# Optimization experiments

Measured on AMD Instinct MI355X. Metric: run time of the kernel, lower is better.

The kernel has to match this reference:

```python
import jax, jax.numpy as jnp
import numpy as np

B, LAT, H, O, T, NPART = 256, 512, 1024, 128, 100, 2


def _lin(x, w, b):
    return x @ w.T + b


def _lrelu(x):
    return jnp.where(x > 0, x, 0.01 * x)


def setup_inputs() -> dict:
    key = jax.random.key(0)
    ks = jax.random.split(key, 32)
    s = 0.02
    def n(k, shape):
        return jax.random.normal(k, shape, dtype=jnp.float32) * s
    return {
        "encoder_outputs": jax.random.normal(ks[0], (B, LAT), dtype=jnp.float32),
        "encoder_hidden": jax.random.normal(ks[1], (B, LAT), dtype=jnp.float32),
        "start_token": jax.random.normal(ks[2], (1, O), dtype=jnp.float32),
        "lat2hid_w": n(ks[3], (H, LAT)), "lat2hid_b": n(ks[4], (H,)),
        "lat2hid2_w": n(ks[5], (H, LAT)), "lat2hid2_b": n(ks[6], (H,)),
        "emb_fc_w": n(ks[7], (H, O)), "emb_fc_b": n(ks[8], (H,)),
        "W_ih": n(ks[9], (4 * H, H)), "W_hh": n(ks[10], (4 * H, H)),
        "b_ih": n(ks[11], (4 * H,)), "b_hh": n(ks[12], (4 * H,)),
        "out_w": n(ks[13], (O, H)), "out_b": n(ks[14], (O,)),
        "fc_seq_w": n(ks[15], (H, LAT)), "fc_seq_b": n(ks[16], (H,)),
        "fc_seq2_w": n(ks[17], (1, H)), "fc_seq2_b": n(ks[18], (1,)),
        "fc_mass_w": n(ks[19], (H, LAT)), "fc_mass_b": n(ks[20], (H,)),
        "fc_mass2_w": n(ks[21], (H, H)), "fc_mass2_b": n(ks[22], (H,)),
        "fc_mass3_w": n(ks[23], (NPART, H)), "fc_mass3_b": n(ks[24], (NPART,)),
        "seq_len": T,
    }


def reference(encoder_outputs, encoder_hidden, start_token,
              lat2hid_w, lat2hid_b, lat2hid2_w, lat2hid2_b,
              emb_fc_w, emb_fc_b, W_ih, W_hh, b_ih, b_hh,
              out_w, out_b, fc_seq_w, fc_seq_b, fc_seq2_w, fc_seq2_b,
              fc_mass_w, fc_mass_b, fc_mass2_w, fc_mass2_b,
              fc_mass3_w, fc_mass3_b, seq_len):
    batch = encoder_hidden.shape[0]
    # initial LSTM state: LeakyReLU(Linear(encoder_hidden))
    h0 = _lrelu(_lin(encoder_hidden, lat2hid_w, lat2hid_b))   # [B,H]
    c0 = _lrelu(_lin(encoder_hidden, lat2hid2_w, lat2hid2_b))  # [B,H]
    # embedded start token, repeated over batch
    x0 = jnp.broadcast_to(_lin(start_token, emb_fc_w, emb_fc_b), (batch, h0.shape[1]))

    def step(carry, _):
        h, c, x = carry
        xr = jax.nn.relu(x)  # forward_step applies relu to the input
        gates = _lin(xr, W_ih, b_ih) + _lin(h, W_hh, b_hh)  # [B,4H], torch gate order i,f,g,o
        i, f, g, o = jnp.split(gates, 4, axis=-1)
        c = jax.nn.sigmoid(f) * c + jax.nn.sigmoid(i) * jnp.tanh(g)
        h = jax.nn.sigmoid(o) * jnp.tanh(c)
        # LSTM output h is fed back as next input (before the `out` projection)
        return (h, c, h), h

    (hT, cT, _), hs = jax.lax.scan(step, (h0, c0, x0), None, length=seq_len)
    decoder_outputs = _lin(hs.transpose(1, 0, 2), out_w, out_b)  # [B,T,O]

    num = jax.nn.relu(_lin(_lrelu(_lin(encoder_outputs, fc_seq_w, fc_seq_b)), fc_seq2_w, fc_seq2_b))  # [B,1]
    m = _lrelu(_lin(encoder_outputs, fc_mass_w, fc_mass_b))
    m = _lrelu(_lin(m, fc_mass2_w, fc_mass2_b))
    mass = jax.nn.softmax(_lin(m, fc_mass3_w, fc_mass3_b), axis=-1)  # [B,num_part]
    return (decoder_outputs, hT[None], cT[None], num, mass)
```

## Files before the change

kernel.cpp:

```cpp
#include <hip/hip_runtime.h>

#define BD 256
#define HD 1024
#define KC 2048
#define LATD 512
#define OD 128
#define TS 100

typedef __attribute__((ext_vector_type(8))) short s16x8;
typedef __attribute__((ext_vector_type(4))) float f32x4;

__device__ __forceinline__ float b2f(short s) {
  return __uint_as_float(((unsigned)(unsigned short)s) << 16);
}
__device__ __forceinline__ short f2b(float f) {
  unsigned u = __float_as_uint(f);
  u += 0x7fff + ((u >> 16) & 1);
  return (short)(u >> 16);
}
__device__ __forceinline__ float sigm(float x) { return 1.f / (1.f + __expf(-x)); }
__device__ __forceinline__ float tanh_f(float x) { return 1.f - 2.f / (__expf(2.f * x) + 1.f); }

__device__ __forceinline__ size_t hf_idx(int m, int kh) {
  int kc = kh >> 3;
  int q2 = kc >> 6, it = (kc >> 2) & 15, qq = kc & 3;
  int mt = m >> 4, r = m & 15;
  return (((size_t)(mt * 32 + q2 * 16 + it)) * 64 + qq * 16 + r) * 8 + (kh & 7);
}

__device__ __forceinline__ s16x8 relu8(s16x8 v) {
  s16x8 o;
#pragma unroll
  for (int e = 0; e < 8; ++e) o[e] = v[e] > 0 ? v[e] : (short)0;
  return o;
}


__global__ __launch_bounds__(256) void cvt8_k(const float* __restrict__ in,
                                              short* __restrict__ out) {
  int i = (blockIdx.x * 256 + threadIdx.x) * 8;
  f32x4 a = *(const f32x4*)(in + i), b = *(const f32x4*)(in + i + 4);
  s16x8 o;
#pragma unroll
  for (int e = 0; e < 4; ++e) { o[e] = f2b(a[e]); o[4 + e] = f2b(b[e]); }
  *(s16x8*)(out + i) = o;
}

__global__ __launch_bounds__(256) void wrep_k(const float* __restrict__ Wih,
                                              const float* __restrict__ Whh,
                                              short* __restrict__ Wt) {
  int i = blockIdx.x * 256 + threadIdx.x;
  int lan = i & 15, quad = (i >> 4) & 3, kit = (i >> 6) & 63, bn = i >> 12;
  int g = bn >> 6, bx = bn & 63;
  int n = g * HD + bx * 16 + lan;
  int k = kit * 32 + quad * 8;
  const float* src = (k < HD) ? (Wih + (size_t)n * HD + k)
                              : (Whh + (size_t)n * HD + (k - HD));
  f32x4 a = *(const f32x4*)src, b = *(const f32x4*)(src + 4);
  s16x8 o;
#pragma unroll
  for (int e = 0; e < 4; ++e) { o[e] = f2b(a[e]); o[4 + e] = f2b(b[e]); }
  *(s16x8*)(Wt + (size_t)i * 8) = o;
}

__global__ __launch_bounds__(256) void bsum_k(const float* __restrict__ bi,
                                              const float* __restrict__ bh,
                                              float* __restrict__ bs) {
  int i = blockIdx.x * 256 + threadIdx.x;
  bs[i] = bi[i] + bh[i];
}

__global__ __launch_bounds__(256) void x0_k(const float* __restrict__ st,
                                            const float* __restrict__ W,
                                            const float* __restrict__ bias,
                                            short* __restrict__ xrow) {
  int j = blockIdx.x * 256 + threadIdx.x;
  float acc = 0.f;
  for (int k = 0; k < OD; ++k) acc += st[k] * W[j * OD + k];
  acc += bias[j];
  xrow[j] = f2b(acc > 0.f ? acc : 0.f);
}

__global__ __launch_bounds__(256) void xg_k(const short* __restrict__ xrow,
                                            const float* __restrict__ Wih,
                                            float* __restrict__ xg) {
  int l = threadIdx.x & 63, w = threadIdx.x >> 6;
  int j = blockIdx.x * 4 + w;
  const float* row = Wih + (size_t)j * HD + l * 16;
  float acc = 0.f;
#pragma unroll
  for (int c = 0; c < 16; ++c) acc += b2f(xrow[l * 16 + c]) * row[c];
  for (int off = 32; off; off >>= 1) acc += __shfl_down(acc, off);
  if (l == 0) xg[j] = acc;
}

__global__ void zero_ctr_k(unsigned* __restrict__ c) { c[threadIdx.x] = 0u; }

template <int K, bool IN_BF16, int MODE>
__global__ __launch_bounds__(256) void fc_mfma(const void* __restrict__ in_,
                                               const float* __restrict__ W,
                                               const float* __restrict__ bias,
                                               void* __restrict__ out_,
                                               int ostride, int ooff) {
  const int tid = threadIdx.x;
  const int w = tid >> 6, lan = tid & 15, quad = (tid & 63) >> 4;
  const int n0 = blockIdx.x * 64;
  const int m0 = blockIdx.y * 64;
  const int arow = m0 + w * 16 + lan;
  f32x4 acc[4] = {};
  for (int k0 = 0; k0 < K; k0 += 32) {
    const int ka = k0 + quad * 8;
    s16x8 af;
    if (IN_BF16) {
      af = *(const s16x8*)((const short*)in_ + arow * K + ka);
    } else {
      const float* ap = (const float*)in_ + arow * K + ka;
      f32x4 a0 = *(const f32x4*)ap, a1 = *(const f32x4*)(ap + 4);
#pragma unroll
      for (int e = 0; e < 4; ++e) { af[e] = f2b(a0[e]); af[4 + e] = f2b(a1[e]); }
    }
#pragma unroll
    for (int nf = 0; nf < 4; ++nf) {
      const float* bp = W + (n0 + nf * 16 + lan) * K + ka;
      f32x4 b0 = *(const f32x4*)bp, b1 = *(const f32x4*)(bp + 4);
      s16x8 bf;
#pragma unroll
      for (int e = 0; e < 4; ++e) { bf[e] = f2b(b0[e]); bf[4 + e] = f2b(b1[e]); }
      acc[nf] = __builtin_amdgcn_mfma_f32_16x16x32_bf16(af, bf, acc[nf], 0, 0, 0);
    }
  }
#pragma unroll
  for (int nf = 0; nf < 4; ++nf) {
    int col = n0 + nf * 16 + lan;
    float bb = bias[col];
#pragma unroll
    for (int j = 0; j < 4; ++j) {
      int m = m0 + w * 16 + quad * 4 + j;
      float v = acc[nf][j] + bb;
      v = v > 0.f ? v : 0.01f * v;
      if (MODE == 0)
        ((float*)out_)[m * 1024 + col] = v;
      else if (MODE == 1)
        ((short*)out_)[m * ostride + ooff + col] = f2b(v);
      else
        ((short*)out_)[hf_idx(m, col)] = f2b(v);
    }
  }
}

__global__ __launch_bounds__(256) void num_k(const float* __restrict__ n1,
                                             const float* __restrict__ w2,
                                             const float* __restrict__ b2,
                                             float* __restrict__ out) {
  int l = threadIdx.x & 63, w = threadIdx.x >> 6;
  int m = blockIdx.x * 4 + w;
  const float* r = n1 + m * HD + l * 16;
  const float* wv = w2 + l * 16;
  float acc = 0.f;
#pragma unroll
  for (int c = 0; c < 4; ++c) {
    f32x4 a = *(const f32x4*)(r + c * 4), b = *(const f32x4*)(wv + c * 4);
#pragma unroll
    for (int e = 0; e < 4; ++e) acc += a[e] * b[e];
  }
  for (int off = 32; off; off >>= 1) acc += __shfl_down(acc, off);
  if (l == 0) {
    float v = acc + b2[0];
    out[m] = v > 0.f ? v : 0.f;
  }
}

__global__ __launch_bounds__(256) void mass_k(const short* __restrict__ m2,
                                              const float* __restrict__ w3,
                                              const float* __restrict__ b3,
                                              float* __restrict__ out) {
  int l = threadIdx.x & 63, w = threadIdx.x >> 6;
  int m = blockIdx.x * 4 + w;
  const short* r = m2 + m * HD + l * 16;
  s16x8 v0 = *(const s16x8*)r, v1 = *(const s16x8*)(r + 8);
  float z0 = 0.f, z1 = 0.f;
#pragma unroll
  for (int e = 0; e < 8; ++e) {
    float a = b2f(v0[e]), b = b2f(v1[e]);
    z0 += a * w3[l * 16 + e] + b * w3[l * 16 + 8 + e];
    z1 += a * w3[HD + l * 16 + e] + b * w3[HD + l * 16 + 8 + e];
  }
  for (int off = 32; off; off >>= 1) {
    z0 += __shfl_down(z0, off);
    z1 += __shfl_down(z1, off);
  }
  if (l == 0) {
    z0 += b3[0]; z1 += b3[1];
    float mx = fmaxf(z0, z1);
    float e0 = __expf(z0 - mx), e1 = __expf(z1 - mx);
    float s = e0 + e1;
    out[m * 2] = e0 / s;
    out[m * 2 + 1] = e1 / s;
  }
}


#define MF(a, b, c) __builtin_amdgcn_mfma_f32_16x16x32_bf16(a, b, c, 0, 0, 0)

typedef __attribute__((address_space(1))) const void gas_void;
typedef __attribute__((address_space(3))) void las_void;

__device__ __forceinline__ void grid_bar(unsigned* slots, unsigned epoch, int bx) {
  asm volatile("s_waitcnt vmcnt(0)" ::: "memory");
  __syncthreads();
  if (threadIdx.x == 0)
    __hip_atomic_store(slots + bx, epoch, __ATOMIC_RELAXED, __HIP_MEMORY_SCOPE_AGENT);
  if (threadIdx.x < 64) {
    while (!__all(__hip_atomic_load(slots + (int)threadIdx.x, __ATOMIC_RELAXED,
                                    __HIP_MEMORY_SCOPE_AGENT) >= epoch))
      __builtin_amdgcn_s_sleep(1);
  }
  __syncthreads();
}

__global__ __launch_bounds__(512, 2) void lstm_persist(
    short* __restrict__ hA, short* __restrict__ hB, const float* __restrict__ cbuf,
    const short* __restrict__ Wt, const float* __restrict__ bsum,
    const float* __restrict__ xg, short* __restrict__ hsC,
    const short* __restrict__ outw, const float* __restrict__ outb,
    float* __restrict__ dout, float* __restrict__ o_h, float* __restrict__ o_c,
    unsigned* ctr, int CH) {
  __shared__ __align__(16) short sm[65536];

  const int tid = threadIdx.x;
  const int w = tid >> 6, l = tid & 63;
  const int w4 = w & 3, gp = w >> 2;
  const int bx = blockIdx.x, by = blockIdx.y;
  const int q = l >> 4, r = l & 15;
  const int q2 = w4 & 1;
  const int sr = (w4 >> 1) + 2 * gp;

  s16x8 W[32];
#pragma unroll
  for (int it = 0; it < 16; ++it)
#pragma unroll
    for (int gi = 0; gi < 2; ++gi) {
      const int g = gp * 2 + gi;
      W[it * 2 + gi] =
          *(const s16x8*)(Wt + (((size_t)(g * 64 + bx) * 64 + w4 * 16 + it) * 64 + l) * 8);
    }
#pragma unroll
  for (int i = 0; i < 32; ++i) asm volatile("" : "+v"(W[i]));

  const int mloc0 = tid >> 4, hc = tid & 15;
  const int chh = bx * 16 + hc;
  const float bs0 = bsum[chh], bs1 = bsum[HD + chh];
  const float bs2 = bsum[2 * HD + chh], bs3 = bsum[3 * HD + chh];
  const float xg0 = xg[chh], xg1 = xg[HD + chh];
  const float xg2 = xg[2 * HD + chh], xg3 = xg[3 * HD + chh];
  int idxA[2];
  size_t hIdx[2];
  float creg[2];
#pragma unroll
  for (int cc2 = 0; cc2 < 2; ++cc2) {
    const int mg = by * 64 + mloc0 + cc2 * 32;
    idxA[cc2] = mg * HD + chh;
    hIdx[cc2] = hf_idx(mg, chh);
    creg[cc2] = cbuf[idxA[cc2]];
  }

  float* red = (float*)sm;
  unsigned* s1 = ctr + by * 128;
  unsigned* s2 = s1 + 64;
  int tslot = 0;
  unsigned pcnt = 0;

  for (int t = 0; t < TS; ++t) {
    const short* src = (t & 1) ? hB : hA;
    short* dst = (t & 1) ? hA : hB;

    f32x4 c00 = {}, c01 = {}, c10 = {}, c11 = {};
    f32x4 c20 = {}, c21 = {}, c30 = {}, c31 = {};

#pragma unroll
    for (int j = 0; j < 16; ++j) {
      const int fi = sr * 16 + j;
      const int it = fi >> 2, mtl = fi & 3;
      const short* g = src + ((size_t)((by * 4 + mtl) * 32 + q2 * 16 + it)) * 512 + (size_t)l * 8;
      __builtin_amdgcn_global_load_lds((gas_void*)g,
                                       (las_void*)(sm + q2 * 32768 + fi * 512), 16, 0, 17);
    }
    asm volatile("s_waitcnt vmcnt(0)" ::: "memory");
    __builtin_amdgcn_s_barrier();

    if (t > 0 || w4 >= 2) {
      const short* cb = sm + q2 * 32768;
#pragma unroll
      for (int it = 0; it < 16; ++it) {
        const short* fb = cb + it * 2048 + l * 8;
        s16x8 a0 = *(const s16x8*)(fb);
        s16x8 a1 = *(const s16x8*)(fb + 512);
        s16x8 a2 = *(const s16x8*)(fb + 1024);
        s16x8 a3 = *(const s16x8*)(fb + 1536);
        if (w4 < 2) { a0 = relu8(a0); a1 = relu8(a1); a2 = relu8(a2); a3 = relu8(a3); }
        const s16x8 w0 = W[it * 2], w1 = W[it * 2 + 1];
        c00 = MF(a0, w0, c00); c01 = MF(a0, w1, c01);
        c10 = MF(a1, w0, c10); c11 = MF(a1, w1, c11);
        c20 = MF(a2, w0, c20); c21 = MF(a2, w1, c21);
        c30 = MF(a3, w0, c30); c31 = MF(a3, w1, c31);
      }
    }
    __builtin_amdgcn_s_barrier();

    {
      float* base = red + (size_t)(w * 64 + l) * 4;
      *(f32x4*)(base + 0 * 2048) = c00;
      *(f32x4*)(base + 1 * 2048) = c01;
      *(f32x4*)(base + 2 * 2048) = c10;
      *(f32x4*)(base + 3 * 2048) = c11;
      *(f32x4*)(base + 4 * 2048) = c20;
      *(f32x4*)(base + 5 * 2048) = c21;
      *(f32x4*)(base + 6 * 2048) = c30;
      *(f32x4*)(base + 7 * 2048) = c31;
    }
    __syncthreads();

#pragma unroll
    for (int cc2 = 0; cc2 < 2; ++cc2) {
      const int mloc = mloc0 + cc2 * 32;
      const int mtl = mloc >> 4, qq = (mloc & 15) >> 2, jj = mloc & 3;
      const int lane = qq * 16 + hc;
      float g4[4];
#pragma unroll
      for (int g = 0; g < 4; ++g) {
        const int s = mtl * 2 + (g & 1);
        const int wv = (g >> 1) * 4;
        float sum = 0.f;
#pragma unroll
        for (int k2 = 0; k2 < 4; ++k2)
          sum += red[(size_t)(s * 512 + (wv + k2) * 64 + lane) * 4 + jj];
        g4[g] = sum;
      }
      float gi_ = g4[0] + bs0;
      float gf = g4[1] + bs1;
      float gg = g4[2] + bs2;
      float go = g4[3] + bs3;
      if (t == 0) { gi_ += xg0; gf += xg1; gg += xg2; go += xg3; }
      float cn = sigm(gf) * creg[cc2] + sigm(gi_) * tanh_f(gg);
      creg[cc2] = cn;
      float h = sigm(go) * tanh_f(cn);
      short h16 = f2b(h);
      __hip_atomic_store(dst + hIdx[cc2], h16, __ATOMIC_RELAXED, __HIP_MEMORY_SCOPE_AGENT);
      __hip_atomic_store(hsC + (size_t)tslot * BD * HD + idxA[cc2], h16,
                         __ATOMIC_RELAXED, __HIP_MEMORY_SCOPE_AGENT);
      if (t == TS - 1) { o_h[idxA[cc2]] = h; o_c[idxA[cc2]] = cn; }
    }
    if (++tslot == CH) tslot = 0;

    grid_bar(s1, (unsigned)(t + 1), bx);

    if (tslot == 0) {
      if (bx < 2 * CH) {
        const int tloc = bx >> 1, nj = bx & 1;
        const int tglob = t + 1 - CH + tloc;
        const short* hsrc = hsC + (size_t)tloc * BD * HD + (size_t)by * 64 * HD;
        const int amt = w & 3, nfh = w >> 2;
        f32x4 p0 = {}, p1 = {};
#pragma unroll
        for (int cc = 0; cc < 2; ++cc) {
#pragma unroll
          for (int j = 0; j < 8; ++j) {
            const int fi = w * 8 + j;
            const int it = fi >> 2, ml = fi & 3;
            const short* g = hsrc + (size_t)(ml * 16 + r) * HD + (cc * 16 + it) * 32 + q * 8;
            __builtin_amdgcn_global_load_lds((gas_void*)g, (las_void*)(sm + fi * 512), 16, 0, 17);
          }
          asm volatile("s_waitcnt vmcnt(0)" ::: "memory");
          __syncthreads();
#pragma unroll
          for (int itl = 0; itl < 16; ++itl) {
            const short* fb = sm + itl * 2048 + amt * 512 + l * 8;
            s16x8 a = *(const s16x8*)(fb);
            const int kk = (cc * 16 + itl) * 32 + q * 8;
            s16x8 b0 = *(const s16x8*)(outw + (size_t)(nj * 64 + nfh * 32 + r) * HD + kk);
            s16x8 b1 = *(const s16x8*)(outw + (size_t)(nj * 64 + nfh * 32 + 16 + r) * HD + kk);
            p0 = MF(a, b0, p0);
            p1 = MF(a, b1, p1);
          }
          __syncthreads();
        }
#pragma unroll
        for (int f2 = 0; f2 < 2; ++f2) {
          const int col = nj * 64 + nfh * 32 + f2 * 16 + r;
          const float bb = outb[col];
          const f32x4 pa = f2 ? p1 : p0;
#pragma unroll
          for (int j2 = 0; j2 < 4; ++j2) {
            const int brow = by * 64 + amt * 16 + q * 4 + j2;
            dout[((size_t)brow * TS + tglob) * OD + col] = pa[j2] + bb;
          }
        }
      }
      ++pcnt;
      grid_bar(s2, pcnt, bx);
    }
  }
}

extern "C" void kernel_launch(void* const* d_in, const int* in_sizes, int n_in,
                              void* d_out, int out_size, void* d_ws, size_t ws_size,
                              hipStream_t stream) {
  static const int exp_sizes[26] = {
      131072, 131072, 128, 524288, 1024, 524288, 1024, 131072, 1024,
      4194304, 4194304, 4096, 4096, 131072, 128, 524288, 1024, 1024, 1,
      524288, 1024, 1048576, 1024, 2048, 2, 1};
  if (n_in < 26) return;
  for (int i = 0; i < 26; ++i)
    if (in_sizes[i] != exp_sizes[i]) return;

  const float* enc_out = (const float*)d_in[0];
  const float* enc_hid = (const float*)d_in[1];
  const float* start_tok = (const float*)d_in[2];
  const float* l2h_w = (const float*)d_in[3];
  const float* l2h_b = (const float*)d_in[4];
  const float* l2h2_w = (const float*)d_in[5];
  const float* l2h2_b = (const float*)d_in[6];
  const float* emb_w = (const float*)d_in[7];
  const float* emb_b = (const float*)d_in[8];
  const float* Wih_f = (const float*)d_in[9];
  const float* Whh_f = (const float*)d_in[10];
  const float* bih = (const float*)d_in[11];
  const float* bhh = (const float*)d_in[12];
  const float* outw_f = (const float*)d_in[13];
  const float* outb = (const float*)d_in[14];
  const float* seq_w = (const float*)d_in[15];
  const float* seq_b = (const float*)d_in[16];
  const float* seq2_w = (const float*)d_in[17];
  const float* seq2_b = (const float*)d_in[18];
  const float* mass_w = (const float*)d_in[19];
  const float* mass_b = (const float*)d_in[20];
  const float* mass2_w = (const float*)d_in[21];
  const float* mass2_b = (const float*)d_in[22];
  const float* mass3_w = (const float*)d_in[23];
  const float* mass3_b = (const float*)d_in[24];

  char* p = (char*)d_ws;
  float* c_buf = (float*)p;  p += (size_t)BD * HD * 4;
  float* bsum = (float*)p;   p += (size_t)4 * HD * 4;
  float* xg = (float*)p;     p += (size_t)4 * HD * 4;
  float* n1 = (float*)p;     p += (size_t)BD * HD * 4;
  short* m1 = (short*)p;     p += (size_t)BD * HD * 2;
  short* m2 = (short*)p;     p += (size_t)BD * HD * 2;
  short* xrow = (short*)p;   p += (size_t)HD * 2;
  short* hA = (short*)p;     p += (size_t)BD * HD * 2;
  short* hB = (short*)p;     p += (size_t)BD * HD * 2;
  short* Wt = (short*)p;     p += (size_t)4 * HD * KC * 2;
  short* outw = (short*)p;   p += (size_t)OD * HD * 2;
  unsigned* ctrs = (unsigned*)p; p += 2048;
  short* hsC = (short*)p;
  size_t fixed_bytes = (size_t)(p - (char*)d_ws);
  const size_t step_bytes = (size_t)BD * HD * 2;
  int CH = 0;
  const int cands[7] = {25, 20, 10, 5, 4, 2, 1};
  for (int ci = 0; ci < 7; ++ci) {
    if (fixed_bytes + (size_t)cands[ci] * step_bytes <= ws_size) { CH = cands[ci]; break; }
  }
  if (CH == 0) return;

  float* dout = (float*)d_out;
  float* o_dec = dout;
  float* o_h = dout + (size_t)BD * TS * OD;
  float* o_c = o_h + (size_t)BD * HD;
  float* o_num = o_c + (size_t)BD * HD;
  float* o_mass = o_num + BD;

  wrep_k<<<4096, 256, 0, stream>>>(Wih_f, Whh_f, Wt);
  cvt8_k<<<OD * HD / 2048, 256, 0, stream>>>(outw_f, outw);
  bsum_k<<<16, 256, 0, stream>>>(bih, bhh, bsum);
  x0_k<<<4, 256, 0, stream>>>(start_tok, emb_w, emb_b, xrow);
  xg_k<<<1024, 256, 0, stream>>>(xrow, Wih_f, xg);
  zero_ctr_k<<<1, 512, 0, stream>>>(ctrs);

  dim3 fcg(16, 4);
  fc_mfma<LATD, false, 2><<<fcg, 256, 0, stream>>>(enc_hid, l2h_w, l2h_b, hA, 0, 0);
  fc_mfma<LATD, false, 0><<<fcg, 256, 0, stream>>>(enc_hid, l2h2_w, l2h2_b, c_buf, 0, 0);
  fc_mfma<LATD, false, 0><<<fcg, 256, 0, stream>>>(enc_out, seq_w, seq_b, n1, 0, 0);
  fc_mfma<LATD, false, 1><<<fcg, 256, 0, stream>>>(enc_out, mass_w, mass_b, m1, HD, 0);
  fc_mfma<HD, true, 1><<<fcg, 256, 0, stream>>>(m1, mass2_w, mass2_b, m2, HD, 0);
  num_k<<<64, 256, 0, stream>>>(n1, seq2_w, seq2_b, o_num);
  mass_k<<<64, 256, 0, stream>>>(m2, mass3_w, mass3_b, o_mass);

  lstm_persist<<<dim3(64, 4), 512, 0, stream>>>(
      hA, hB, c_buf, Wt, bsum, xg, hsC, outw, outb, o_dec, o_h, o_c, ctrs, CH);
}
```

Baseline: 1.410 ms.

## Double LSTM persistent block to 1024 threads and split h load into two halves

The persistent LSTM kernel now runs 1024 threads per block. Each wave holds 16 weight fragments instead of 32 and owns a single gate and a single batch row per thread in the elementwise stage, which halves per-thread register pressure and MFMA chains. The h-state staging into LDS is split so the first half of the MFMA loop starts after a partial vmcnt wait while the rest still loads, overlapping load latency with compute. The output projection is rebalanced to one accumulator per wave. The risks are an extra block barrier per step and the cost of syncing a larger block.

```diff
diff --git a/kernel.cpp b/kernel.cpp
--- a/kernel.cpp
+++ b/kernel.cpp
@@ -218,7 +218,7 @@
   __syncthreads();
 }
 
-__global__ __launch_bounds__(512, 2) void lstm_persist(
+__global__ __launch_bounds__(1024, 4) void lstm_persist(
     short* __restrict__ hA, short* __restrict__ hB, const float* __restrict__ cbuf,
     const short* __restrict__ Wt, const float* __restrict__ bsum,
     const float* __restrict__ xg, short* __restrict__ hsC,
@@ -229,40 +229,31 @@
 
   const int tid = threadIdx.x;
   const int w = tid >> 6, l = tid & 63;
-  const int w4 = w & 3, gp = w >> 2;
+  const int w4q = w >> 2, g = w & 3;
   const int bx = blockIdx.x, by = blockIdx.y;
   const int q = l >> 4, r = l & 15;
-  const int q2 = w4 & 1;
-  const int sr = (w4 >> 1) + 2 * gp;
-
-  s16x8 W[32];
+  const int q2 = w4q & 1;
+  const int sr8 = (w4q >> 1) * 4 + g;
+
+  s16x8 W[16];
 #pragma unroll
   for (int it = 0; it < 16; ++it)
-#pragma unroll
-    for (int gi = 0; gi < 2; ++gi) {
-      const int g = gp * 2 + gi;
-      W[it * 2 + gi] =
-          *(const s16x8*)(Wt + (((size_t)(g * 64 + bx) * 64 + w4 * 16 + it) * 64 + l) * 8);
-    }
-#pragma unroll
-  for (int i = 0; i < 32; ++i) asm volatile("" : "+v"(W[i]));
-
-  const int mloc0 = tid >> 4, hc = tid & 15;
+    W[it] = *(const s16x8*)(Wt + (((size_t)(g * 64 + bx) * 64 + w4q * 16 + it) * 64 + l) * 8);
+#pragma unroll
+  for (int i = 0; i < 16; ++i) asm volatile("" : "+v"(W[i]));
+
+  const int mloc = tid >> 4, hc = tid & 15;
   const int chh = bx * 16 + hc;
   const float bs0 = bsum[chh], bs1 = bsum[HD + chh];
   const float bs2 = bsum[2 * HD + chh], bs3 = bsum[3 * HD + chh];
   const float xg0 = xg[chh], xg1 = xg[HD + chh];
   const float xg2 = xg[2 * HD + chh], xg3 = xg[3 * HD + chh];
-  int idxA[2];
-  size_t hIdx[2];
-  float creg[2];
-#pragma unroll
-  for (int cc2 = 0; cc2 < 2; ++cc2) {
-    const int mg = by * 64 + mloc0 + cc2 * 32;
-    idxA[cc2] = mg * HD + chh;
-    hIdx[cc2] = hf_idx(mg, chh);
-    creg[cc2] = cbuf[idxA[cc2]];
-  }
+  const int mg = by * 64 + mloc;
+  const int idxA = mg * HD + chh;
+  const size_t hIdx = hf_idx(mg, chh);
+  float creg = cbuf[idxA];
+  const int mtlE = mloc >> 4, qqE = (mloc & 15) >> 2, jjE = mloc & 3;
+  const int laneE = qqE * 16 + hc;
 
   float* red = (float*)sm;
   unsigned* s1 = ctr + by * 128;
@@ -274,81 +265,81 @@
     const short* src = (t & 1) ? hB : hA;
     short* dst = (t & 1) ? hA : hB;
 
-    f32x4 c00 = {}, c01 = {}, c10 = {}, c11 = {};
-    f32x4 c20 = {}, c21 = {}, c30 = {}, c31 = {};
-
-#pragma unroll
-    for (int j = 0; j < 16; ++j) {
-      const int fi = sr * 16 + j;
+    f32x4 c0 = {}, c1 = {}, c2 = {}, c3 = {};
+
+#pragma unroll
+    for (int j = 0; j < 8; ++j) {
+      const int fi = j * 8 + sr8;
       const int it = fi >> 2, mtl = fi & 3;
-      const short* g = src + ((size_t)((by * 4 + mtl) * 32 + q2 * 16 + it)) * 512 + (size_t)l * 8;
-      __builtin_amdgcn_global_load_lds((gas_void*)g,
+      const short* gp = src + ((size_t)((by * 4 + mtl) * 32 + q2 * 16 + it)) * 512 + (size_t)l * 8;
+      __builtin_amdgcn_global_load_lds((gas_void*)gp,
                                        (las_void*)(sm + q2 * 32768 + fi * 512), 16, 0, 17);
     }
-    asm volatile("s_waitcnt vmcnt(0)" ::: "memory");
+
+    const short* cb = sm + q2 * 32768;
+    asm volatile("s_waitcnt vmcnt(4)" ::: "memory");
     __builtin_amdgcn_s_barrier();
-
-    if (t > 0 || w4 >= 2) {
-      const short* cb = sm + q2 * 32768;
-#pragma unroll
-      for (int it = 0; it < 16; ++it) {
+    if (t > 0 || w4q >= 2) {
+#pragma unroll
+      for (int it = 0; it < 8; ++it) {
         const short* fb = cb + it * 2048 + l * 8;
         s16x8 a0 = *(const s16x8*)(fb);
         s16x8 a1 = *(const s16x8*)(fb + 512);
         s16x8 a2 = *(const s16x8*)(fb + 1024);
         s16x8 a3 = *(const s16x8*)(fb + 1536);
-        if (w4 < 2) { a0 = relu8(a0); a1 = relu8(a1); a2 = relu8(a2); a3 = relu8(a3); }
-        const s16x8 w0 = W[it * 2], w1 = W[it * 2 + 1];
-        c00 = MF(a0, w0, c00); c01 = MF(a0, w1, c01);
-        c10 = MF(a1, w0, c10); c11 = MF(a1, w1, c11);
-        c20 = MF(a2, w0, c20); c21 = MF(a2, w1, c21);
-        c30 = MF(a3, w0, c30); c31 = MF(a3, w1, c31);
+        if (w4q < 2) { a0 = relu8(a0); a1 = relu8(a1); a2 = relu8(a2); a3 = relu8(a3); }
+        const s16x8 wf = W[it];
+        c0 = MF(a0, wf, c0); c1 = MF(a1, wf, c1);
+        c2 = MF(a2, wf, c2); c3 = MF(a3, wf, c3);
       }
     }
+    asm volatile("s_waitcnt vmcnt(0)" ::: "memory");
     __builtin_amdgcn_s_barrier();
+    if (t > 0 || w4q >= 2) {
+#pragma unroll
+      for (int it = 8; it < 16; ++it) {
+        const short* fb = cb + it * 2048 + l * 8;
+        s16x8 a0 = *(const s16x8*)(fb);
+        s16x8 a1 = *(const s16x8*)(fb + 512);
+        s16x8 a2 = *(const s16x8*)(fb + 1024);
+        s16x8 a3 = *(const s16x8*)(fb + 1536);
+        if (w4q < 2) { a0 = relu8(a0); a1 = relu8(a1); a2 = relu8(a2); a3 = relu8(a3); }
+        const s16x8 wf = W[it];
+        c0 = MF(a0, wf, c0); c1 = MF(a1, wf, c1);
+        c2 = MF(a2, wf, c2); c3 = MF(a3, wf, c3);
+      }
+    }
+    __builtin_amdgcn_s_barrier();
+
+    *(f32x4*)(red + ((size_t)((0 * 4 + g) * 4 + w4q) * 64 + l) * 4) = c0;
+    *(f32x4*)(red + ((size_t)((1 * 4 + g) * 4 + w4q) * 64 + l) * 4) = c1;
+    *(f32x4*)(red + ((size_t)((2 * 4 + g) * 4 + w4q) * 64 + l) * 4) = c2;
+    *(f32x4*)(red + ((size_t)((3 * 4 + g) * 4 + w4q) * 64 + l) * 4) = c3;
+    __syncthreads();
 
     {
-      float* base = red + (size_t)(w * 64 + l) * 4;
-      *(f32x4*)(base + 0 * 2048) = c00;
-      *(f32x4*)(base + 1 * 2048) = c01;
-      *(f32x4*)(base + 2 * 2048) = c10;
-      *(f32x4*)(base + 3 * 2048) = c11;
-      *(f32x4*)(base + 4 * 2048) = c20;
-      *(f32x4*)(base + 5 * 2048) = c21;
-      *(f32x4*)(base + 6 * 2048) = c30;
-      *(f32x4*)(base + 7 * 2048) = c31;
-    }
-    __syncthreads();
-
-#pragma unroll
-    for (int cc2 = 0; cc2 < 2; ++cc2) {
-      const int mloc = mloc0 + cc2 * 32;
-      const int mtl = mloc >> 4, qq = (mloc & 15) >> 2, jj = mloc & 3;
-      const int lane = qq * 16 + hc;
       float g4[4];
 #pragma unroll
-      for (int g = 0; g < 4; ++g) {
-        const int s = mtl * 2 + (g & 1);
-        const int wv = (g >> 1) * 4;
+      for (int gg = 0; gg < 4; ++gg) {
         float sum = 0.f;
 #pragma unroll
         for (int k2 = 0; k2 < 4; ++k2)
-          sum += red[(size_t)(s * 512 + (wv + k2) * 64 + lane) * 4 + jj];
-        g4[g] = sum;
+          sum += red[((size_t)((mtlE * 4 + gg) * 4 + k2) * 64 + laneE) * 4 + jjE];
+        g4[gg] = sum;
       }
       float gi_ = g4[0] + bs0;
       float gf = g4[1] + bs1;
-      float gg = g4[2] + bs2;
+      float gg2 = g4[2] + bs2;
       float go = g4[3] + bs3;
-      if (t == 0) { gi_ += xg0; gf += xg1; gg += xg2; go += xg3; }
-      float cn = sigm(gf) * creg[cc2] + sigm(gi_) * tanh_f(gg);
-      creg[cc2] = cn;
+      if (t == 0) { gi_ += xg0; gf += xg1; gg2 += xg2; go += xg3; }
+      float cn = sigm(gf) * creg + sigm(gi_) * tanh_f(gg2);
+      creg = cn;
       float h = sigm(go) * tanh_f(cn);
       short h16 = f2b(h);
-      __hip_atomic_store(dst + hIdx[cc2], h16, __ATOMIC_RELAXED, __HIP_MEMORY_SCOPE_AGENT);
-      __hip_atomic_store(hsC + (size_t)tslot * BD * HD + idxA[cc2], h16,
+      __hip_atomic_store(dst + hIdx, h16, __ATOMIC_RELAXED, __HIP_MEMORY_SCOPE_AGENT);
+      __hip_atomic_store(hsC + (size_t)tslot * BD * HD + idxA, h16,
                          __ATOMIC_RELAXED, __HIP_MEMORY_SCOPE_AGENT);
-      if (t == TS - 1) { o_h[idxA[cc2]] = h; o_c[idxA[cc2]] = cn; }
+      if (t == TS - 1) { o_h[idxA] = h; o_c[idxA] = cn; }
     }
     if (++tslot == CH) tslot = 0;
 
@@ -360,15 +351,14 @@
         const int tglob = t + 1 - CH + tloc;
         const short* hsrc = hsC + (size_t)tloc * BD * HD + (size_t)by * 64 * HD;
         const int amt = w & 3, nfh = w >> 2;
-        f32x4 p0 = {}, p1 = {};
+        f32x4 p0 = {};
 #pragma unroll
         for (int cc = 0; cc < 2; ++cc) {
 #pragma unroll
-          for (int j = 0; j < 8; ++j) {
-            const int fi = w * 8 + j;
-            const int it = fi >> 2, ml = fi & 3;
-            const short* g = hsrc + (size_t)(ml * 16 + r) * HD + (cc * 16 + it) * 32 + q * 8;
-            __builtin_amdgcn_global_load_lds((gas_void*)g, (las_void*)(sm + fi * 512), 16, 0, 17);
+          for (int j = 0; j < 4; ++j) {
+            const int fi = w * 4 + j;
+            const short* gp = hsrc + (size_t)(j * 16 + r) * HD + (cc * 16 + w) * 32 + q * 8;
+            __builtin_amdgcn_global_load_lds((gas_void*)gp, (las_void*)(sm + fi * 512), 16, 0, 17);
           }
           asm volatile("s_waitcnt vmcnt(0)" ::: "memory");
           __syncthreads();
@@ -377,22 +367,18 @@
             const short* fb = sm + itl * 2048 + amt * 512 + l * 8;
             s16x8 a = *(const s16x8*)(fb);
             const int kk = (cc * 16 + itl) * 32 + q * 8;
-            s16x8 b0 = *(const s16x8*)(outw + (size_t)(nj * 64 + nfh * 32 + r) * HD + kk);
-            s16x8 b1 = *(const s16x8*)(outw + (size_t)(nj * 64 + nfh * 32 + 16 + r) * HD + kk);
+            s16x8 b0 = *(const s16x8*)(outw + (size_t)(nj * 64 + nfh * 16 + r) * HD + kk);
             p0 = MF(a, b0, p0);
-            p1 = MF(a, b1, p1);
           }
           __syncthreads();
         }
-#pragma unroll
-        for (int f2 = 0; f2 < 2; ++f2) {
-          const int col = nj * 64 + nfh * 32 + f2 * 16 + r;
+        {
+          const int col = nj * 64 + nfh * 16 + r;
           const float bb = outb[col];
-          const f32x4 pa = f2 ? p1 : p0;
 #pragma unroll
           for (int j2 = 0; j2 < 4; ++j2) {
             const int brow = by * 64 + amt * 16 + q * 4 + j2;
-            dout[((size_t)brow * TS + tglob) * OD + col] = pa[j2] + bb;
+            dout[((size_t)brow * TS + tglob) * OD + col] = p0[j2] + bb;
           }
         }
       }
@@ -485,6 +471,6 @@
   num_k<<<64, 256, 0, stream>>>(n1, seq2_w, seq2_b, o_num);
   mass_k<<<64, 256, 0, stream>>>(m2, mass3_w, mass3_b, o_mass);
 
-  lstm_persist<<<dim3(64, 4), 512, 0, stream>>>(
+  lstm_persist<<<dim3(64, 4), 1024, 0, stream>>>(
       hA, hB, c_buf, Wt, bsum, xg, hsC, outw, outb, o_dec, o_h, o_c, ctrs, CH);
 }
```

New measurement: 1.584 ms. 1.12x slower.

## Use a ring buffer for hidden states, flag-based grid barrier, and fuse prep kernels

Applied to the files above, without the earlier changes.

Replaces the ping-pong h buffers plus the separate history buffer with a single ring of CH+1 hidden-state slots. The output projection now reads h directly from the ring in its tiled layout, which removes the duplicate per-step store of h. The grid barrier changes from every block polling all 64 slots to block 0 polling and then publishing one flag that the other blocks poll. The many small setup kernels are merged into fewer launches (prep_small, fc_heads, num_mass_k), cutting launch overhead. The trade-off is an extra hop in each barrier, plus ring-slot reuse that depends on the projection finishing before a slot is overwritten.

```diff
diff --git a/kernel.cpp b/kernel.cpp
--- a/kernel.cpp
+++ b/kernel.cpp
@@ -35,16 +35,6 @@
   return o;
 }
 
-
-__global__ __launch_bounds__(256) void cvt8_k(const float* __restrict__ in,
-                                              short* __restrict__ out) {
-  int i = (blockIdx.x * 256 + threadIdx.x) * 8;
-  f32x4 a = *(const f32x4*)(in + i), b = *(const f32x4*)(in + i + 4);
-  s16x8 o;
-#pragma unroll
-  for (int e = 0; e < 4; ++e) { o[e] = f2b(a[e]); o[4 + e] = f2b(b[e]); }
-  *(s16x8*)(out + i) = o;
-}
 
 __global__ __launch_bounds__(256) void wrep_k(const float* __restrict__ Wih,
                                               const float* __restrict__ Whh,
@@ -63,22 +53,33 @@
   *(s16x8*)(Wt + (size_t)i * 8) = o;
 }
 
-__global__ __launch_bounds__(256) void bsum_k(const float* __restrict__ bi,
-                                              const float* __restrict__ bh,
-                                              float* __restrict__ bs) {
-  int i = blockIdx.x * 256 + threadIdx.x;
-  bs[i] = bi[i] + bh[i];
-}
-
-__global__ __launch_bounds__(256) void x0_k(const float* __restrict__ st,
-                                            const float* __restrict__ W,
-                                            const float* __restrict__ bias,
-                                            short* __restrict__ xrow) {
-  int j = blockIdx.x * 256 + threadIdx.x;
-  float acc = 0.f;
-  for (int k = 0; k < OD; ++k) acc += st[k] * W[j * OD + k];
-  acc += bias[j];
-  xrow[j] = f2b(acc > 0.f ? acc : 0.f);
+__global__ __launch_bounds__(256) void prep_small(
+    const float* __restrict__ bi, const float* __restrict__ bh, float* __restrict__ bs,
+    const float* __restrict__ st, const float* __restrict__ embW,
+    const float* __restrict__ embB, short* __restrict__ xrow,
+    unsigned* __restrict__ ctrs,
+    const float* __restrict__ outw_f, short* __restrict__ outw) {
+  const int b = blockIdx.x, tid = threadIdx.x;
+  if (b < 16) {
+    int i = b * 256 + tid;
+    bs[i] = bi[i] + bh[i];
+  } else if (b < 20) {
+    int j = (b - 16) * 256 + tid;
+    float acc = 0.f;
+    for (int k = 0; k < OD; ++k) acc += st[k] * embW[j * OD + k];
+    acc += embB[j];
+    xrow[j] = f2b(acc > 0.f ? acc : 0.f);
+  } else if (b == 20) {
+#pragma unroll
+    for (int e = 0; e < 4; ++e) ctrs[tid * 4 + e] = 0u;
+  } else {
+    int i = ((b - 21) * 256 + tid) * 8;
+    f32x4 a = *(const f32x4*)(outw_f + i), c = *(const f32x4*)(outw_f + i + 4);
+    s16x8 o;
+#pragma unroll
+    for (int e = 0; e < 4; ++e) { o[e] = f2b(a[e]); o[4 + e] = f2b(c[e]); }
+    *(s16x8*)(outw + i) = o;
+  }
 }
 
 __global__ __launch_bounds__(256) void xg_k(const short* __restrict__ xrow,
@@ -94,38 +95,38 @@
   if (l == 0) xg[j] = acc;
 }
 
-__global__ void zero_ctr_k(unsigned* __restrict__ c) { c[threadIdx.x] = 0u; }
-
-template <int K, bool IN_BF16, int MODE>
-__global__ __launch_bounds__(256) void fc_mfma(const void* __restrict__ in_,
-                                               const float* __restrict__ W,
-                                               const float* __restrict__ bias,
-                                               void* __restrict__ out_,
-                                               int ostride, int ooff) {
+__global__ __launch_bounds__(256) void fc_heads(
+    const float* __restrict__ enc_hid, const float* __restrict__ enc_out,
+    const float* __restrict__ w0, const float* __restrict__ b0,
+    const float* __restrict__ w1, const float* __restrict__ b1,
+    const float* __restrict__ w2, const float* __restrict__ b2,
+    const float* __restrict__ w3, const float* __restrict__ b3,
+    short* __restrict__ ring, float* __restrict__ cbuf,
+    float* __restrict__ n1, short* __restrict__ m1) {
+  const int z = blockIdx.z;
+  const float* in_ = (z <= 1) ? enc_hid : enc_out;
+  const float* W = (z == 0) ? w0 : (z == 1) ? w1 : (z == 2) ? w2 : w3;
+  const float* bias = (z == 0) ? b0 : (z == 1) ? b1 : (z == 2) ? b2 : b3;
   const int tid = threadIdx.x;
   const int w = tid >> 6, lan = tid & 15, quad = (tid & 63) >> 4;
   const int n0 = blockIdx.x * 64;
   const int m0 = blockIdx.y * 64;
   const int arow = m0 + w * 16 + lan;
   f32x4 acc[4] = {};
-  for (int k0 = 0; k0 < K; k0 += 32) {
+  for (int k0 = 0; k0 < LATD; k0 += 32) {
     const int ka = k0 + quad * 8;
     s16x8 af;
-    if (IN_BF16) {
-      af = *(const s16x8*)((const short*)in_ + arow * K + ka);
-    } else {
-      const float* ap = (const float*)in_ + arow * K + ka;
-      f32x4 a0 = *(const f32x4*)ap, a1 = *(const f32x4*)(ap + 4);
-#pragma unroll
-      for (int e = 0; e < 4; ++e) { af[e] = f2b(a0[e]); af[4 + e] = f2b(a1[e]); }
-    }
+    const float* ap = in_ + (size_t)arow * LATD + ka;
+    f32x4 a0 = *(const f32x4*)ap, a1 = *(const f32x4*)(ap + 4);
+#pragma unroll
+    for (int e = 0; e < 4; ++e) { af[e] = f2b(a0[e]); af[4 + e] = f2b(a1[e]); }
 #pragma unroll
     for (int nf = 0; nf < 4; ++nf) {
-      const float* bp = W + (n0 + nf * 16 + lan) * K + ka;
-      f32x4 b0 = *(const f32x4*)bp, b1 = *(const f32x4*)(bp + 4);
+      const float* bp = W + (size_t)(n0 + nf * 16 + lan) * LATD + ka;
+      f32x4 b0v = *(const f32x4*)bp, b1v = *(const f32x4*)(bp + 4);
       s16x8 bf;
 #pragma unroll
-      for (int e = 0; e < 4; ++e) { bf[e] = f2b(b0[e]); bf[4 + e] = f2b(b1[e]); }
+      for (int e = 0; e < 4; ++e) { bf[e] = f2b(b0v[e]); bf[4 + e] = f2b(b1v[e]); }
       acc[nf] = __builtin_amdgcn_mfma_f32_16x16x32_bf16(af, bf, acc[nf], 0, 0, 0);
     }
   }
@@ -138,64 +139,95 @@
       int m = m0 + w * 16 + quad * 4 + j;
       float v = acc[nf][j] + bb;
       v = v > 0.f ? v : 0.01f * v;
-      if (MODE == 0)
-        ((float*)out_)[m * 1024 + col] = v;
-      else if (MODE == 1)
-        ((short*)out_)[m * ostride + ooff + col] = f2b(v);
-      else
-        ((short*)out_)[hf_idx(m, col)] = f2b(v);
-    }
-  }
-}
-
-__global__ __launch_bounds__(256) void num_k(const float* __restrict__ n1,
-                                             const float* __restrict__ w2,
-                                             const float* __restrict__ b2,
-                                             float* __restrict__ out) {
+      if (z == 0)      ring[hf_idx(m, col)] = f2b(v);
+      else if (z == 1) cbuf[m * HD + col] = v;
+      else if (z == 2) n1[m * HD + col] = v;
+      else             m1[m * HD + col] = f2b(v);
+    }
+  }
+}
+
+__global__ __launch_bounds__(256) void fc_mass2(const short* __restrict__ in_,
+                                                const float* __restrict__ W,
+                                                const float* __restrict__ bias,
+                                                short* __restrict__ out_) {
+  const int tid = threadIdx.x;
+  const int w = tid >> 6, lan = tid & 15, quad = (tid & 63) >> 4;
+  const int n0 = blockIdx.x * 64;
+  const int m0 = blockIdx.y * 64;
+  const int arow = m0 + w * 16 + lan;
+  f32x4 acc[4] = {};
+  for (int k0 = 0; k0 < HD; k0 += 32) {
+    const int ka = k0 + quad * 8;
+    s16x8 af = *(const s16x8*)(in_ + (size_t)arow * HD + ka);
+#pragma unroll
+    for (int nf = 0; nf < 4; ++nf) {
+      const float* bp = W + (size_t)(n0 + nf * 16 + lan) * HD + ka;
+      f32x4 b0v = *(const f32x4*)bp, b1v = *(const f32x4*)(bp + 4);
+      s16x8 bf;
+#pragma unroll
+      for (int e = 0; e < 4; ++e) { bf[e] = f2b(b0v[e]); bf[4 + e] = f2b(b1v[e]); }
+      acc[nf] = __builtin_amdgcn_mfma_f32_16x16x32_bf16(af, bf, acc[nf], 0, 0, 0);
+    }
+  }
+#pragma unroll
+  for (int nf = 0; nf < 4; ++nf) {
+    int col = n0 + nf * 16 + lan;
+    float bb = bias[col];
+#pragma unroll
+    for (int j = 0; j < 4; ++j) {
+      int m = m0 + w * 16 + quad * 4 + j;
+      float v = acc[nf][j] + bb;
+      v = v > 0.f ? v : 0.01f * v;
+      out_[(size_t)m * HD + col] = f2b(v);
+    }
+  }
+}
+
+__global__ __launch_bounds__(256) void num_mass_k(
+    const float* __restrict__ n1, const float* __restrict__ w2, const float* __restrict__ b2,
+    float* __restrict__ onum, const short* __restrict__ m2,
+    const float* __restrict__ w3, const float* __restrict__ b3, float* __restrict__ omass) {
   int l = threadIdx.x & 63, w = threadIdx.x >> 6;
-  int m = blockIdx.x * 4 + w;
-  const float* r = n1 + m * HD + l * 16;
-  const float* wv = w2 + l * 16;
-  float acc = 0.f;
-#pragma unroll
-  for (int c = 0; c < 4; ++c) {
-    f32x4 a = *(const f32x4*)(r + c * 4), b = *(const f32x4*)(wv + c * 4);
-#pragma unroll
-    for (int e = 0; e < 4; ++e) acc += a[e] * b[e];
-  }
-  for (int off = 32; off; off >>= 1) acc += __shfl_down(acc, off);
-  if (l == 0) {
-    float v = acc + b2[0];
-    out[m] = v > 0.f ? v : 0.f;
-  }
-}
-
-__global__ __launch_bounds__(256) void mass_k(const short* __restrict__ m2,
-                                              const float* __restrict__ w3,
-                                              const float* __restrict__ b3,
-                                              float* __restrict__ out) {
-  int l = threadIdx.x & 63, w = threadIdx.x >> 6;
-  int m = blockIdx.x * 4 + w;
-  const short* r = m2 + m * HD + l * 16;
-  s16x8 v0 = *(const s16x8*)r, v1 = *(const s16x8*)(r + 8);
-  float z0 = 0.f, z1 = 0.f;
-#pragma unroll
-  for (int e = 0; e < 8; ++e) {
-    float a = b2f(v0[e]), b = b2f(v1[e]);
-    z0 += a * w3[l * 16 + e] + b * w3[l * 16 + 8 + e];
-    z1 += a * w3[HD + l * 16 + e] + b * w3[HD + l * 16 + 8 + e];
-  }
-  for (int off = 32; off; off >>= 1) {
-    z0 += __shfl_down(z0, off);
-    z1 += __shfl_down(z1, off);
-  }
-  if (l == 0) {
-    z0 += b3[0]; z1 += b3[1];
-    float mx = fmaxf(z0, z1);
-    float e0 = __expf(z0 - mx), e1 = __expf(z1 - mx);
-    float s = e0 + e1;
-    out[m * 2] = e0 / s;
-    out[m * 2 + 1] = e1 / s;
+  if (blockIdx.x < 64) {
+    int m = blockIdx.x * 4 + w;
+    const float* r = n1 + (size_t)m * HD + l * 16;
+    const float* wv = w2 + l * 16;
+    float acc = 0.f;
+#pragma unroll
+    for (int c = 0; c < 4; ++c) {
+      f32x4 a = *(const f32x4*)(r + c * 4), b = *(const f32x4*)(wv + c * 4);
+#pragma unroll
+      for (int e = 0; e < 4; ++e) acc += a[e] * b[e];
+    }
+    for (int off = 32; off; off >>= 1) acc += __shfl_down(acc, off);
+    if (l == 0) {
+      float v = acc + b2[0];
+      onum[m] = v > 0.f ? v : 0.f;
+    }
+  } else {
+    int m = (blockIdx.x - 64) * 4 + w;
+    const short* r = m2 + (size_t)m * HD + l * 16;
+    s16x8 v0 = *(const s16x8*)r, v1 = *(const s16x8*)(r + 8);
+    float z0 = 0.f, z1 = 0.f;
+#pragma unroll
+    for (int e = 0; e < 8; ++e) {
+      float a = b2f(v0[e]), b = b2f(v1[e]);
+      z0 += a * w3[l * 16 + e] + b * w3[l * 16 + 8 + e];
+      z1 += a * w3[HD + l * 16 + e] + b * w3[HD + l * 16 + 8 + e];
+    }
+    for (int off = 32; off; off >>= 1) {
+      z0 += __shfl_down(z0, off);
+      z1 += __shfl_down(z1, off);
+    }
+    if (l == 0) {
+      z0 += b3[0]; z1 += b3[1];
+      float mx = fmaxf(z0, z1);
+      float e0 = __expf(z0 - mx), e1 = __expf(z1 - mx);
+      float s = e0 + e1;
+      omass[m * 2] = e0 / s;
+      omass[m * 2 + 1] = e1 / s;
+    }
   }
 }
 
@@ -205,26 +237,35 @@
 typedef __attribute__((address_space(1))) const void gas_void;
 typedef __attribute__((address_space(3))) void las_void;
 
-__device__ __forceinline__ void grid_bar(unsigned* slots, unsigned epoch, int bx) {
+__device__ __forceinline__ void grid_bar(unsigned* slots, unsigned* flag,
+                                         unsigned epoch, int bx) {
   asm volatile("s_waitcnt vmcnt(0)" ::: "memory");
   __syncthreads();
-  if (threadIdx.x == 0)
+  const int tid = threadIdx.x;
+  if (tid == 0)
     __hip_atomic_store(slots + bx, epoch, __ATOMIC_RELAXED, __HIP_MEMORY_SCOPE_AGENT);
-  if (threadIdx.x < 64) {
-    while (!__all(__hip_atomic_load(slots + (int)threadIdx.x, __ATOMIC_RELAXED,
-                                    __HIP_MEMORY_SCOPE_AGENT) >= epoch))
-      __builtin_amdgcn_s_sleep(1);
+  if (bx == 0) {
+    if (tid < 64) {
+      while (!__all(__hip_atomic_load(slots + tid, __ATOMIC_RELAXED,
+                                      __HIP_MEMORY_SCOPE_AGENT) >= epoch))
+        __builtin_amdgcn_s_sleep(2);
+      if (tid == 0)
+        __hip_atomic_store(flag, epoch, __ATOMIC_RELAXED, __HIP_MEMORY_SCOPE_AGENT);
+    }
+  } else if (tid == 0) {
+    while (__hip_atomic_load(flag, __ATOMIC_RELAXED, __HIP_MEMORY_SCOPE_AGENT) < epoch)
+      __builtin_amdgcn_s_sleep(2);
   }
   __syncthreads();
 }
 
 __global__ __launch_bounds__(512, 2) void lstm_persist(
-    short* __restrict__ hA, short* __restrict__ hB, const float* __restrict__ cbuf,
+    short* __restrict__ ring, const float* __restrict__ cbuf,
     const short* __restrict__ Wt, const float* __restrict__ bsum,
-    const float* __restrict__ xg, short* __restrict__ hsC,
+    const float* __restrict__ xg,
     const short* __restrict__ outw, const float* __restrict__ outb,
     float* __restrict__ dout, float* __restrict__ o_h, float* __restrict__ o_c,
-    unsigned* ctr, int CH) {
+    unsigned* ctr, int CH, int R) {
   __shared__ __align__(16) short sm[65536];
 
   const int tid = threadIdx.x;
@@ -264,15 +305,19 @@
     creg[cc2] = cbuf[idxA[cc2]];
   }
 
+  const size_t BUFSZ = (size_t)BD * HD;
   float* red = (float*)sm;
-  unsigned* s1 = ctr + by * 128;
-  unsigned* s2 = s1 + 64;
+  unsigned* cbase = ctr + by * 256;
+  unsigned* s1 = cbase;
+  unsigned* f1 = cbase + 80;
+  unsigned* s2 = cbase + 128;
+  unsigned* f2g = cbase + 208;
   int tslot = 0;
   unsigned pcnt = 0;
 
   for (int t = 0; t < TS; ++t) {
-    const short* src = (t & 1) ? hB : hA;
-    short* dst = (t & 1) ? hA : hB;
+    const short* src = ring + (size_t)(t % R) * BUFSZ;
+    short* dst = ring + (size_t)((t + 1) % R) * BUFSZ;
 
     f32x4 c00 = {}, c01 = {}, c10 = {}, c11 = {};
     f32x4 c20 = {}, c21 = {}, c30 = {}, c31 = {};
@@ -346,19 +391,17 @@
       float h = sigm(go) * tanh_f(cn);
       short h16 = f2b(h);
       __hip_atomic_store(dst + hIdx[cc2], h16, __ATOMIC_RELAXED, __HIP_MEMORY_SCOPE_AGENT);
-      __hip_atomic_store(hsC + (size_t)tslot * BD * HD + idxA[cc2], h16,
-                         __ATOMIC_RELAXED, __HIP_MEMORY_SCOPE_AGENT);
       if (t == TS - 1) { o_h[idxA[cc2]] = h; o_c[idxA[cc2]] = cn; }
     }
     if (++tslot == CH) tslot = 0;
 
-    grid_bar(s1, (unsigned)(t + 1), bx);
+    grid_bar(s1, f1, (unsigned)(t + 1), bx);
 
     if (tslot == 0) {
       if (bx < 2 * CH) {
         const int tloc = bx >> 1, nj = bx & 1;
         const int tglob = t + 1 - CH + tloc;
-        const short* hsrc = hsC + (size_t)tloc * BD * HD + (size_t)by * 64 * HD;
+        const short* hsrc = ring + (size_t)((tglob + 1) % R) * BUFSZ;
         const int amt = w & 3, nfh = w >> 2;
         f32x4 p0 = {}, p1 = {};
 #pragma unroll
@@ -367,7 +410,7 @@
           for (int j = 0; j < 8; ++j) {
             const int fi = w * 8 + j;
             const int it = fi >> 2, ml = fi & 3;
-            const short* g = hsrc + (size_t)(ml * 16 + r) * HD + (cc * 16 + it) * 32 + q * 8;
+            const short* g = hsrc + ((size_t)((by * 4 + ml) * 32 + cc * 16 + it)) * 512 + (size_t)l * 8;
             __builtin_amdgcn_global_load_lds((gas_void*)g, (las_void*)(sm + fi * 512), 16, 0, 17);
           }
           asm volatile("s_waitcnt vmcnt(0)" ::: "memory");
@@ -397,7 +440,7 @@
         }
       }
       ++pcnt;
-      grid_bar(s2, pcnt, bx);
+      grid_bar(s2, f2g, pcnt, bx);
     }
   }
 }
@@ -447,18 +490,16 @@
   short* m1 = (short*)p;     p += (size_t)BD * HD * 2;
   short* m2 = (short*)p;     p += (size_t)BD * HD * 2;
   short* xrow = (short*)p;   p += (size_t)HD * 2;
-  short* hA = (short*)p;     p += (size_t)BD * HD * 2;
-  short* hB = (short*)p;     p += (size_t)BD * HD * 2;
   short* Wt = (short*)p;     p += (size_t)4 * HD * KC * 2;
   short* outw = (short*)p;   p += (size_t)OD * HD * 2;
-  unsigned* ctrs = (unsigned*)p; p += 2048;
-  short* hsC = (short*)p;
+  unsigned* ctrs = (unsigned*)p; p += 4096;
+  short* ring = (short*)p;
   size_t fixed_bytes = (size_t)(p - (char*)d_ws);
   const size_t step_bytes = (size_t)BD * HD * 2;
   int CH = 0;
   const int cands[7] = {25, 20, 10, 5, 4, 2, 1};
   for (int ci = 0; ci < 7; ++ci) {
-    if (fixed_bytes + (size_t)cands[ci] * step_bytes <= ws_size) { CH = cands[ci]; break; }
+    if (fixed_bytes + (size_t)(cands[ci] + 1) * step_bytes <= ws_size) { CH = cands[ci]; break; }
   }
   if (CH == 0) return;
 
@@ -470,21 +511,16 @@
   float* o_mass = o_num + BD;
 
   wrep_k<<<4096, 256, 0, stream>>>(Wih_f, Whh_f, Wt);
-  cvt8_k<<<OD * HD / 2048, 256, 0, stream>>>(outw_f, outw);
-  bsum_k<<<16, 256, 0, stream>>>(bih, bhh, bsum);
-  x0_k<<<4, 256, 0, stream>>>(start_tok, emb_w, emb_b, xrow);
+  prep_small<<<85, 256, 0, stream>>>(bih, bhh, bsum, start_tok, emb_w, emb_b,
+                                     xrow, ctrs, outw_f, outw);
   xg_k<<<1024, 256, 0, stream>>>(xrow, Wih_f, xg);
-  zero_ctr_k<<<1, 512, 0, stream>>>(ctrs);
-
-  dim3 fcg(16, 4);
-  fc_mfma<LATD, false, 2><<<fcg, 256, 0, stream>>>(enc_hid, l2h_w, l2h_b, hA, 0, 0);
-  fc_mfma<LATD, false, 0><<<fcg, 256, 0, stream>>>(enc_hid, l2h2_w, l2h2_b, c_buf, 0, 0);
-  fc_mfma<LATD, false, 0><<<fcg, 256, 0, stream>>>(enc_out, seq_w, seq_b, n1, 0, 0);
-  fc_mfma<LATD, false, 1><<<fcg, 256, 0, stream>>>(enc_out, mass_w, mass_b, m1, HD, 0);
-  fc_mfma<HD, true, 1><<<fcg, 256, 0, stream>>>(m1, mass2_w, mass2_b, m2, HD, 0);
-  num_k<<<64, 256, 0, stream>>>(n1, seq2_w, seq2_b, o_num);
-  mass_k<<<64, 256, 0, stream>>>(m2, mass3_w, mass3_b, o_mass);
+
+  fc_heads<<<dim3(16, 4, 4), 256, 0, stream>>>(
+      enc_hid, enc_out, l2h_w, l2h_b, l2h2_w, l2h2_b, seq_w, seq_b, mass_w, mass_b,
+      ring, c_buf, n1, m1);
+  fc_mass2<<<dim3(16, 4), 256, 0, stream>>>(m1, mass2_w, mass2_b, m2);
+  num_mass_k<<<128, 256, 0, stream>>>(n1, seq2_w, seq2_b, o_num, m2, mass3_w, mass3_b, o_mass);
 
   lstm_persist<<<dim3(64, 4), 512, 0, stream>>>(
-      hA, hB, c_buf, Wt, bsum, xg, hsC, outw, outb, o_dec, o_h, o_c, ctrs, CH);
-}
+      ring, c_buf, Wt, bsum, xg, outw, outb, o_dec, o_h, o_c, ctrs, CH, CH + 1);
+}
```

Result: faster. 1.177 ms (-16.5%).
